# Kernel optimization log

Measured on AMD Instinct MI355X. Metric: run time of the kernel, lower is better.

The kernel has to match this reference:

```python
import jax, jax.numpy as jnp
import numpy as np

# SMPL-style 22-joint kinematic tree; parents[i] < i for i >= 2 as the module's loop requires.
PARENTS = np.array([-1, 0, 0, 0, 1, 2, 3, 4, 5, 6, 7, 8, 9, 9, 9, 12, 13, 14, 16, 17, 18, 19])
L, J, D6 = 65536, 22, 6


def cont6d_to_mat(d6):
    """6D continuous rotation -> 3x3 rotation matrix (Gram-Schmidt). Columns are b1,b2,b3."""
    a1, a2 = d6[..., :3], d6[..., 3:]
    b1 = a1 / jnp.maximum(jnp.linalg.norm(a1, axis=-1, keepdims=True), 1e-12)
    b2 = a2 - b1 * jnp.sum(b1 * a2, axis=-1, keepdims=True)
    b2 = b2 / jnp.maximum(jnp.linalg.norm(b2, axis=-1, keepdims=True), 1e-12)
    b3 = jnp.cross(b1, b2)
    return jnp.stack((b1, b2, b3), axis=-1)  # (..., 3, 3)


def setup_inputs() -> dict:
    key = jax.random.key(0)
    k1, k2 = jax.random.split(key)
    pred_series = jax.random.normal(k1, (L, J, D6), dtype=jnp.float32)
    offsets = 0.1 * jax.random.normal(k2, (J, 3), dtype=jnp.float32)  # bone offsets (buffer)
    return {"pred_series": pred_series, "offsets": offsets}


def reference(pred_series, offsets):
    # pred_series: (L, 22, 6) -> global positions (L, 22, 3)
    rot_mats = cont6d_to_mat(pred_series)          # (L, 22, 3, 3)

    # Cumulative root rotation: R_t = R_{t-1} @ delta_t, R_{-1} = I  (sequential scan over time)
    deltas = rot_mats[:, 1]                        # (L, 3, 3)
    def step(R, d):
        Rn = R @ d
        return Rn, Rn
    _, R = jax.lax.scan(step, jnp.eye(3, dtype=pred_series.dtype), deltas)  # (L, 3, 3)

    # Root translation: integrate rotated local velocities
    vel_local = pred_series[:, 0, :3]              # (L, 3)
    global_vel = jnp.einsum('tij,tj->ti', R, vel_local)
    root_pos = jnp.cumsum(global_vel, axis=0)      # (L, 3)

    # FK down the static tree, vectorized over time; unrolled over 22 joints (static).
    rots = [None] * J
    pos = [None] * J
    rots[0], pos[0] = R, root_pos
    rots[1] = R
    pos[1] = pos[0] + jnp.einsum('tij,j->ti', R, offsets[1])
    for i in range(2, J):
        p = int(PARENTS[i])
        rots[i] = jnp.einsum('tij,tjk->tik', rots[p], rot_mats[:, i])
        pos[i] = pos[p] + jnp.einsum('tij,j->ti', rots[p], offsets[i])
    return jnp.stack(pos, axis=1)                  # (L, 22, 3)
```

## Files before the change

### kernel.cpp

```cpp
#include <hip/hip_runtime.h>
#include <stdint.h>


#define LTOT 65536
#define ROW 132
#define P1B 256
#define NSCB (LTOT / P1B)

struct Aff { float A[9]; float b[3]; };

__device__ __forceinline__ void d6_to_mat(float a0, float a1, float a2,
                                          float a3, float a4, float a5,
                                          float R[9]) {
  float n1 = sqrtf(a0 * a0 + a1 * a1 + a2 * a2);
  float i1 = 1.0f / fmaxf(n1, 1e-12f);
  float b10 = a0 * i1, b11 = a1 * i1, b12 = a2 * i1;
  float d = b10 * a3 + b11 * a4 + b12 * a5;
  float c0 = a3 - d * b10, c1 = a4 - d * b11, c2 = a5 - d * b12;
  float n2 = sqrtf(c0 * c0 + c1 * c1 + c2 * c2);
  float i2 = 1.0f / fmaxf(n2, 1e-12f);
  float b20 = c0 * i2, b21 = c1 * i2, b22 = c2 * i2;
  float b30 = b11 * b22 - b12 * b21;
  float b31 = b12 * b20 - b10 * b22;
  float b32 = b10 * b21 - b11 * b20;
  R[0] = b10; R[1] = b20; R[2] = b30;
  R[3] = b11; R[4] = b21; R[5] = b31;
  R[6] = b12; R[7] = b22; R[8] = b32;
}

__device__ __forceinline__ void mat_mul(const float A[9], const float B[9], float C[9]) {
#pragma unroll
  for (int i = 0; i < 3; ++i)
#pragma unroll
    for (int j = 0; j < 3; ++j)
      C[i * 3 + j] = A[i * 3 + 0] * B[0 + j] + A[i * 3 + 1] * B[3 + j] + A[i * 3 + 2] * B[6 + j];
}

__device__ __forceinline__ void mat_vec(const float A[9], float x, float y, float z,
                                        float& ox, float& oy, float& oz) {
  ox = A[0] * x + A[1] * y + A[2] * z;
  oy = A[3] * x + A[4] * y + A[5] * z;
  oz = A[6] * x + A[7] * y + A[8] * z;
}

__device__ __forceinline__ void compose(const Aff& P, const Aff& T, Aff& O) {
  mat_mul(P.A, T.A, O.A);
  float bx, by, bz;
  mat_vec(P.A, T.b[0], T.b[1], T.b[2], bx, by, bz);
  O.b[0] = P.b[0] + bx; O.b[1] = P.b[1] + by; O.b[2] = P.b[2] + bz;
}

__device__ __forceinline__ void aff_identity(Aff& v) {
  v.A[0] = 1.f; v.A[1] = 0.f; v.A[2] = 0.f;
  v.A[3] = 0.f; v.A[4] = 1.f; v.A[5] = 0.f;
  v.A[6] = 0.f; v.A[7] = 0.f; v.A[8] = 1.f;
  v.b[0] = 0.f; v.b[1] = 0.f; v.b[2] = 0.f;
}

__device__ __forceinline__ void wave_scan(Aff& v, int lane) {
#pragma unroll
  for (int s = 1; s < 64; s <<= 1) {
    Aff u;
#pragma unroll
    for (int k = 0; k < 9; ++k) u.A[k] = __shfl_up(v.A[k], s, 64);
#pragma unroll
    for (int k = 0; k < 3; ++k) u.b[k] = __shfl_up(v.b[k], s, 64);
    if (lane >= s) { Aff t; compose(u, v, t); v = t; }
  }
}

__device__ __forceinline__ void elem_transform(const float* __restrict__ pred,
                                               int t, Aff& v) {
  const float4* q4 = (const float4*)(pred + (size_t)t * ROW);
  float4 qa = q4[0];
  float4 qb = q4[1];
  float4 qc = q4[2];
  d6_to_mat(qb.z, qb.w, qc.x, qc.y, qc.z, qc.w, v.A);
  mat_vec(v.A, qa.x, qa.y, qa.z, v.b[0], v.b[1], v.b[2]);
}

__global__ __launch_bounds__(P1B) void fk_agg(const float* __restrict__ pred,
                                              float* __restrict__ agg) {
  int tid = threadIdx.x;
  int t = blockIdx.x * P1B + tid;
  int lane = tid & 63, wid = tid >> 6;
  Aff v;
  elem_transform(pred, t, v);
  wave_scan(v, lane);
  __shared__ float sagg[P1B / 64][12];
  if (lane == 63) {
#pragma unroll
    for (int k = 0; k < 9; ++k) sagg[wid][k] = v.A[k];
#pragma unroll
    for (int k = 0; k < 3; ++k) sagg[wid][9 + k] = v.b[k];
  }
  __syncthreads();
  if (tid == P1B - 1) {
    Aff pre; aff_identity(pre);
    for (int w = 0; w < P1B / 64 - 1; ++w) {
      Aff g, t2;
#pragma unroll
      for (int k = 0; k < 9; ++k) g.A[k] = sagg[w][k];
#pragma unroll
      for (int k = 0; k < 3; ++k) g.b[k] = sagg[w][9 + k];
      compose(pre, g, t2); pre = t2;
    }
    Aff f; compose(pre, v, f);
    float4* a = (float4*)(agg + (size_t)blockIdx.x * 12);
    a[0] = make_float4(f.A[0], f.A[1], f.A[2], f.A[3]);
    a[1] = make_float4(f.A[4], f.A[5], f.A[6], f.A[7]);
    a[2] = make_float4(f.A[8], f.b[0], f.b[1], f.b[2]);
  }
}

struct Rowv { float2 a, b, c; };
__device__ __forceinline__ Rowv loadrow(const float* q, int j) {
  const float2* p = (const float2*)(q + j * 6);
  Rowv r; r.a = p[0]; r.b = p[1]; r.c = p[2]; return r;
}
__device__ __forceinline__ void rowmat(const Rowv& r, float M[9]) {
  d6_to_mat(r.a.x, r.a.y, r.b.x, r.b.y, r.c.x, r.c.y, M);
}
__device__ __forceinline__ void childp(const float* Rp, const float* offs, int j,
                                       float px, float py, float pz,
                                       float& ox, float& oy, float& oz,
                                       float* ob) {
  float dx, dy, dz;
  mat_vec(Rp, offs[j * 3], offs[j * 3 + 1], offs[j * 3 + 2], dx, dy, dz);
  ox = px + dx; oy = py + dy; oz = pz + dz;
  ob[j * 3] = ox; ob[j * 3 + 1] = oy; ob[j * 3 + 2] = oz;
}

__global__ __launch_bounds__(1024) void fk_main(const float* __restrict__ pred,
                                                const float* __restrict__ offs,
                                                const float* __restrict__ agg,
                                                float* __restrict__ out) {
  int x = threadIdx.x;
  int y = threadIdx.y;
  int z = threadIdx.z;
  int b = blockIdx.x;

  __shared__ float sagg1[4][12];
  __shared__ float sagg2[4][12];
  __shared__ float ebuf[12];
  __shared__ float sg[P1B][13];

  int tl = z * 64 + x;
  int t = b * P1B + tl;
  const float* q = pred + (size_t)t * ROW;
  float* ob = out + (size_t)t * 66;

  Rowv w0, w1, w2, w3, w4, w5, w6, w7, w8;
  if (y == 0) {
    w0 = loadrow(q, 4); w1 = loadrow(q, 7);
  } else if (y == 1) {
    w0 = loadrow(q, 2); w1 = loadrow(q, 5); w2 = loadrow(q, 8);
  } else if (y == 2) {
    w0 = loadrow(q, 3); w1 = loadrow(q, 6); w2 = loadrow(q, 9);
    w3 = loadrow(q, 12);
  } else {
    w0 = loadrow(q, 3); w1 = loadrow(q, 6); w2 = loadrow(q, 9);
    w3 = loadrow(q, 13); w4 = loadrow(q, 16); w5 = loadrow(q, 18);
    w6 = loadrow(q, 14); w7 = loadrow(q, 17); w8 = loadrow(q, 19);
  }

  int s = x + 64 * y;
  Aff v, f;
  Aff v2, incl;
  if (z == 0) {
    elem_transform(pred, b * P1B + s, v);
    wave_scan(v, x);
    if (x == 63) {
#pragma unroll
      for (int k = 0; k < 9; ++k) sagg1[y][k] = v.A[k];
#pragma unroll
      for (int k = 0; k < 3; ++k) sagg1[y][9 + k] = v.b[k];
    }
  } else if (z == 1) {
    const float4* a = (const float4*)(agg + (size_t)s * 12);
    float4 a0 = a[0], a1 = a[1], a2 = a[2];
    v2.A[0] = a0.x; v2.A[1] = a0.y; v2.A[2] = a0.z; v2.A[3] = a0.w;
    v2.A[4] = a1.x; v2.A[5] = a1.y; v2.A[6] = a1.z; v2.A[7] = a1.w;
    v2.A[8] = a2.x; v2.b[0] = a2.y; v2.b[1] = a2.z; v2.b[2] = a2.w;
    wave_scan(v2, x);
    if (x == 63) {
#pragma unroll
      for (int k = 0; k < 9; ++k) sagg2[y][k] = v2.A[k];
#pragma unroll
      for (int k = 0; k < 3; ++k) sagg2[y][9 + k] = v2.b[k];
    }
  }
  __syncthreads();

  if (z == 0) {
    Aff pre; aff_identity(pre);
    for (int w = 0; w < y; ++w) {
      Aff gg, t2;
#pragma unroll
      for (int k = 0; k < 9; ++k) gg.A[k] = sagg1[w][k];
#pragma unroll
      for (int k = 0; k < 3; ++k) gg.b[k] = sagg1[w][9 + k];
      compose(pre, gg, t2); pre = t2;
    }
    compose(pre, v, f);
  } else if (z == 1) {
    Aff pre; aff_identity(pre);
    for (int w = 0; w < y; ++w) {
      Aff gg, t2;
#pragma unroll
      for (int k = 0; k < 9; ++k) gg.A[k] = sagg2[w][k];
#pragma unroll
      for (int k = 0; k < 3; ++k) gg.b[k] = sagg2[w][9 + k];
      compose(pre, gg, t2); pre = t2;
    }
    compose(pre, v2, incl);
    if (s == b - 1) {
#pragma unroll
      for (int k = 0; k < 9; ++k) ebuf[k] = incl.A[k];
#pragma unroll
      for (int k = 0; k < 3; ++k) ebuf[9 + k] = incl.b[k];
    }
  }
  __syncthreads();

  if (z == 0) {
    Aff eb;
    if (b == 0) aff_identity(eb);
    else {
#pragma unroll
      for (int k = 0; k < 9; ++k) eb.A[k] = ebuf[k];
#pragma unroll
      for (int k = 0; k < 3; ++k) eb.b[k] = ebuf[9 + k];
    }
    Aff g; compose(eb, f, g);
#pragma unroll
    for (int k = 0; k < 9; ++k) sg[s][k] = g.A[k];
#pragma unroll
    for (int k = 0; k < 3; ++k) sg[s][9 + k] = g.b[k];
  }
  __syncthreads();

  float R[9];
#pragma unroll
  for (int k = 0; k < 9; ++k) R[k] = sg[tl][k];
  float px = sg[tl][9], py = sg[tl][10], pz = sg[tl][11];

  float M[9], ra[9], rb[9];
  if (y == 0) {
    ob[0] = px; ob[1] = py; ob[2] = pz;
    float p1x, p1y, p1z, p4x, p4y, p4z, p7x, p7y, p7z, dx, dy, dz;
    childp(R, offs, 1, px, py, pz, p1x, p1y, p1z, ob);
    childp(R, offs, 4, p1x, p1y, p1z, p4x, p4y, p4z, ob);
    rowmat(w0, M); mat_mul(R, M, ra);
    childp(ra, offs, 7, p4x, p4y, p4z, p7x, p7y, p7z, ob);
    rowmat(w1, M); mat_mul(ra, M, rb);
    childp(rb, offs, 10, p7x, p7y, p7z, dx, dy, dz, ob);
  } else if (y == 1) {
    float p2x, p2y, p2z, p5x, p5y, p5z, p8x, p8y, p8z, dx, dy, dz;
    childp(R, offs, 2, px, py, pz, p2x, p2y, p2z, ob);
    rowmat(w0, M); mat_mul(R, M, ra);
    childp(ra, offs, 5, p2x, p2y, p2z, p5x, p5y, p5z, ob);
    rowmat(w1, M); mat_mul(ra, M, rb);
    childp(rb, offs, 8, p5x, p5y, p5z, p8x, p8y, p8z, ob);
    rowmat(w2, M); mat_mul(rb, M, ra);
    childp(ra, offs, 11, p8x, p8y, p8z, dx, dy, dz, ob);
  } else if (y == 2) {
    float p3x, p3y, p3z, p6x, p6y, p6z, p9x, p9y, p9z;
    float p12x, p12y, p12z, dx, dy, dz;
    childp(R, offs, 3, px, py, pz, p3x, p3y, p3z, ob);
    rowmat(w0, M); mat_mul(R, M, ra);
    childp(ra, offs, 6, p3x, p3y, p3z, p6x, p6y, p6z, ob);
    rowmat(w1, M); mat_mul(ra, M, rb);
    childp(rb, offs, 9, p6x, p6y, p6z, p9x, p9y, p9z, ob);
    rowmat(w2, M); mat_mul(rb, M, ra);
    childp(ra, offs, 12, p9x, p9y, p9z, p12x, p12y, p12z, ob);
    rowmat(w3, M); mat_mul(ra, M, rb);
    childp(rb, offs, 15, p12x, p12y, p12z, dx, dy, dz, ob);
  } else {
    float p3x, p3y, p3z, p6x, p6y, p6z, p9x, p9y, p9z, dx, dy, dz;
    mat_vec(R, offs[9], offs[10], offs[11], dx, dy, dz);
    p3x = px + dx; p3y = py + dy; p3z = pz + dz;
    rowmat(w0, M); mat_mul(R, M, ra);
    mat_vec(ra, offs[18], offs[19], offs[20], dx, dy, dz);
    p6x = p3x + dx; p6y = p3y + dy; p6z = p3z + dz;
    rowmat(w1, M); mat_mul(ra, M, rb);
    mat_vec(rb, offs[27], offs[28], offs[29], dx, dy, dz);
    p9x = p6x + dx; p9y = p6y + dy; p9z = p6z + dz;
    rowmat(w2, M); mat_mul(rb, M, ra);
    float r9s[9];
#pragma unroll
    for (int k = 0; k < 9; ++k) r9s[k] = ra[k];
    float pAx, pAy, pAz, pBx, pBy, pBz, pCx, pCy, pCz;
    childp(r9s, offs, 13, p9x, p9y, p9z, pAx, pAy, pAz, ob);
    rowmat(w3, M); mat_mul(r9s, M, rb);
    childp(rb, offs, 16, pAx, pAy, pAz, pBx, pBy, pBz, ob);
    rowmat(w4, M); mat_mul(rb, M, ra);
    childp(ra, offs, 18, pBx, pBy, pBz, pCx, pCy, pCz, ob);
    rowmat(w5, M); mat_mul(ra, M, rb);
    childp(rb, offs, 20, pCx, pCy, pCz, dx, dy, dz, ob);
    childp(r9s, offs, 14, p9x, p9y, p9z, pAx, pAy, pAz, ob);
    rowmat(w6, M); mat_mul(r9s, M, rb);
    childp(rb, offs, 17, pAx, pAy, pAz, pBx, pBy, pBz, ob);
    rowmat(w7, M); mat_mul(rb, M, ra);
    childp(ra, offs, 19, pBx, pBy, pBz, pCx, pCy, pCz, ob);
    rowmat(w8, M); mat_mul(ra, M, rb);
    childp(rb, offs, 21, pCx, pCy, pCz, dx, dy, dz, ob);
  }
}

extern "C" void kernel_launch(void* const* d_in, const int* in_sizes, int n_in,
                              void* d_out, int out_size, void* d_ws, size_t ws_size,
                              hipStream_t stream) {
  const float* pred = (const float*)d_in[0];
  const float* offs = (const float*)d_in[1];
  float* out = (float*)d_out;
  float* agg = (float*)d_ws;

  fk_agg<<<NSCB, P1B, 0, stream>>>(pred, agg);
  fk_main<<<NSCB, dim3(64, 4, 4), 0, stream>>>(pred, offs, agg, out);
}
```

Measured before the change: 97.45 us.

## Fuse aggregate and main kernels into a single-pass scan with inter-block flags

Removes the separate aggregate kernel. Each block now publishes its own 256-step affine aggregate to workspace, then sets a release flag. Later blocks spin on the flags of all earlier blocks and scan those aggregates to get their prefix. This saves a launch and a second pass over the input rows. The cost is spin-waiting that assumes all earlier blocks are resident or scheduled first. The flags are never reset between calls, so a later call can see a stale flag from an earlier call and read stale aggregates.

```diff
diff --git a/kernel.cpp b/kernel.cpp
--- a/kernel.cpp
+++ b/kernel.cpp
@@ -6,6 +6,7 @@
 #define ROW 132
 #define P1B 256
 #define NSCB (LTOT / P1B)
+#define MAGIC 0x13579BDF
 
 struct Aff { float A[9]; float b[3]; };
 
@@ -79,40 +80,6 @@
   mat_vec(v.A, qa.x, qa.y, qa.z, v.b[0], v.b[1], v.b[2]);
 }
 
-__global__ __launch_bounds__(P1B) void fk_agg(const float* __restrict__ pred,
-                                              float* __restrict__ agg) {
-  int tid = threadIdx.x;
-  int t = blockIdx.x * P1B + tid;
-  int lane = tid & 63, wid = tid >> 6;
-  Aff v;
-  elem_transform(pred, t, v);
-  wave_scan(v, lane);
-  __shared__ float sagg[P1B / 64][12];
-  if (lane == 63) {
-#pragma unroll
-    for (int k = 0; k < 9; ++k) sagg[wid][k] = v.A[k];
-#pragma unroll
-    for (int k = 0; k < 3; ++k) sagg[wid][9 + k] = v.b[k];
-  }
-  __syncthreads();
-  if (tid == P1B - 1) {
-    Aff pre; aff_identity(pre);
-    for (int w = 0; w < P1B / 64 - 1; ++w) {
-      Aff g, t2;
-#pragma unroll
-      for (int k = 0; k < 9; ++k) g.A[k] = sagg[w][k];
-#pragma unroll
-      for (int k = 0; k < 3; ++k) g.b[k] = sagg[w][9 + k];
-      compose(pre, g, t2); pre = t2;
-    }
-    Aff f; compose(pre, v, f);
-    float4* a = (float4*)(agg + (size_t)blockIdx.x * 12);
-    a[0] = make_float4(f.A[0], f.A[1], f.A[2], f.A[3]);
-    a[1] = make_float4(f.A[4], f.A[5], f.A[6], f.A[7]);
-    a[2] = make_float4(f.A[8], f.b[0], f.b[1], f.b[2]);
-  }
-}
-
 struct Rowv { float2 a, b, c; };
 __device__ __forceinline__ Rowv loadrow(const float* q, int j) {
   const float2* p = (const float2*)(q + j * 6);
@@ -131,10 +98,11 @@
   ob[j * 3] = ox; ob[j * 3 + 1] = oy; ob[j * 3 + 2] = oz;
 }
 
-__global__ __launch_bounds__(1024) void fk_main(const float* __restrict__ pred,
-                                                const float* __restrict__ offs,
-                                                const float* __restrict__ agg,
-                                                float* __restrict__ out) {
+__global__ __launch_bounds__(1024) void fk_fused(const float* __restrict__ pred,
+                                                 const float* __restrict__ offs,
+                                                 float* __restrict__ agg,
+                                                 int* __restrict__ flags,
+                                                 float* __restrict__ out) {
   int x = threadIdx.x;
   int y = threadIdx.y;
   int z = threadIdx.z;
@@ -147,6 +115,7 @@
 
   int tl = z * 64 + x;
   int t = b * P1B + tl;
+  int s = x + 64 * y;
   const float* q = pred + (size_t)t * ROW;
   float* ob = out + (size_t)t * 66;
 
@@ -164,9 +133,7 @@
     w6 = loadrow(q, 14); w7 = loadrow(q, 17); w8 = loadrow(q, 19);
   }
 
-  int s = x + 64 * y;
-  Aff v, f;
-  Aff v2, incl;
+  Aff v;
   if (z == 0) {
     elem_transform(pred, b * P1B + s, v);
     wave_scan(v, x);
@@ -176,22 +143,10 @@
 #pragma unroll
       for (int k = 0; k < 3; ++k) sagg1[y][9 + k] = v.b[k];
     }
-  } else if (z == 1) {
-    const float4* a = (const float4*)(agg + (size_t)s * 12);
-    float4 a0 = a[0], a1 = a[1], a2 = a[2];
-    v2.A[0] = a0.x; v2.A[1] = a0.y; v2.A[2] = a0.z; v2.A[3] = a0.w;
-    v2.A[4] = a1.x; v2.A[5] = a1.y; v2.A[6] = a1.z; v2.A[7] = a1.w;
-    v2.A[8] = a2.x; v2.b[0] = a2.y; v2.b[1] = a2.z; v2.b[2] = a2.w;
-    wave_scan(v2, x);
-    if (x == 63) {
-#pragma unroll
-      for (int k = 0; k < 9; ++k) sagg2[y][k] = v2.A[k];
-#pragma unroll
-      for (int k = 0; k < 3; ++k) sagg2[y][9 + k] = v2.b[k];
-    }
   }
   __syncthreads();
 
+  Aff v2;
   if (z == 0) {
     Aff pre; aff_identity(pre);
     for (int w = 0; w < y; ++w) {
@@ -202,8 +157,45 @@
       for (int k = 0; k < 3; ++k) gg.b[k] = sagg1[w][9 + k];
       compose(pre, gg, t2); pre = t2;
     }
-    compose(pre, v, f);
+    Aff f; compose(pre, v, f);
+#pragma unroll
+    for (int k = 0; k < 9; ++k) sg[s][k] = f.A[k];
+#pragma unroll
+    for (int k = 0; k < 3; ++k) sg[s][9 + k] = f.b[k];
+    if (s == P1B - 1) {
+      float4* a = (float4*)(agg + (size_t)b * 12);
+      a[0] = make_float4(f.A[0], f.A[1], f.A[2], f.A[3]);
+      a[1] = make_float4(f.A[4], f.A[5], f.A[6], f.A[7]);
+      a[2] = make_float4(f.A[8], f.b[0], f.b[1], f.b[2]);
+      __threadfence();
+      __hip_atomic_store(&flags[b], MAGIC, __ATOMIC_RELEASE,
+                         __HIP_MEMORY_SCOPE_AGENT);
+    }
   } else if (z == 1) {
+    if (s < b) {
+      while (__hip_atomic_load(&flags[s], __ATOMIC_ACQUIRE,
+                               __HIP_MEMORY_SCOPE_AGENT) != MAGIC) {
+        __builtin_amdgcn_s_sleep(1);
+      }
+      const float4* a = (const float4*)(agg + (size_t)s * 12);
+      float4 a0 = a[0], a1 = a[1], a2 = a[2];
+      v2.A[0] = a0.x; v2.A[1] = a0.y; v2.A[2] = a0.z; v2.A[3] = a0.w;
+      v2.A[4] = a1.x; v2.A[5] = a1.y; v2.A[6] = a1.z; v2.A[7] = a1.w;
+      v2.A[8] = a2.x; v2.b[0] = a2.y; v2.b[1] = a2.z; v2.b[2] = a2.w;
+    } else {
+      aff_identity(v2);
+    }
+    wave_scan(v2, x);
+    if (x == 63) {
+#pragma unroll
+      for (int k = 0; k < 9; ++k) sagg2[y][k] = v2.A[k];
+#pragma unroll
+      for (int k = 0; k < 3; ++k) sagg2[y][9 + k] = v2.b[k];
+    }
+  }
+  __syncthreads();
+
+  if (z == 1 && b > 0 && s == b - 1) {
     Aff pre; aff_identity(pre);
     for (int w = 0; w < y; ++w) {
       Aff gg, t2;
@@ -213,37 +205,30 @@
       for (int k = 0; k < 3; ++k) gg.b[k] = sagg2[w][9 + k];
       compose(pre, gg, t2); pre = t2;
     }
-    compose(pre, v2, incl);
-    if (s == b - 1) {
-#pragma unroll
-      for (int k = 0; k < 9; ++k) ebuf[k] = incl.A[k];
-#pragma unroll
-      for (int k = 0; k < 3; ++k) ebuf[9 + k] = incl.b[k];
-    }
+    Aff incl; compose(pre, v2, incl);
+#pragma unroll
+    for (int k = 0; k < 9; ++k) ebuf[k] = incl.A[k];
+#pragma unroll
+    for (int k = 0; k < 3; ++k) ebuf[9 + k] = incl.b[k];
   }
   __syncthreads();
 
-  if (z == 0) {
-    Aff eb;
-    if (b == 0) aff_identity(eb);
-    else {
-#pragma unroll
-      for (int k = 0; k < 9; ++k) eb.A[k] = ebuf[k];
-#pragma unroll
-      for (int k = 0; k < 3; ++k) eb.b[k] = ebuf[9 + k];
-    }
-    Aff g; compose(eb, f, g);
-#pragma unroll
-    for (int k = 0; k < 9; ++k) sg[s][k] = g.A[k];
-#pragma unroll
-    for (int k = 0; k < 3; ++k) sg[s][9 + k] = g.b[k];
-  }
-  __syncthreads();
-
-  float R[9];
-#pragma unroll
-  for (int k = 0; k < 9; ++k) R[k] = sg[tl][k];
-  float px = sg[tl][9], py = sg[tl][10], pz = sg[tl][11];
+  Aff eb;
+  if (b == 0) aff_identity(eb);
+  else {
+#pragma unroll
+    for (int k = 0; k < 9; ++k) eb.A[k] = ebuf[k];
+#pragma unroll
+    for (int k = 0; k < 3; ++k) eb.b[k] = ebuf[9 + k];
+  }
+  Aff fl;
+#pragma unroll
+  for (int k = 0; k < 9; ++k) fl.A[k] = sg[tl][k];
+#pragma unroll
+  for (int k = 0; k < 3; ++k) fl.b[k] = sg[tl][9 + k];
+  Aff g; compose(eb, fl, g);
+  const float* R = g.A;
+  float px = g.b[0], py = g.b[1], pz = g.b[2];
 
   float M[9], ra[9], rb[9];
   if (y == 0) {
@@ -315,7 +300,7 @@
   const float* offs = (const float*)d_in[1];
   float* out = (float*)d_out;
   float* agg = (float*)d_ws;
-
-  fk_agg<<<NSCB, P1B, 0, stream>>>(pred, agg);
-  fk_main<<<NSCB, dim3(64, 4, 4), 0, stream>>>(pred, offs, agg, out);
-}
+  int* flags = (int*)((char*)d_ws + 16384);
+
+  fk_fused<<<NSCB, dim3(64, 4, 4), 0, stream>>>(pred, offs, agg, flags, out);
+}
```

After: 135.9 us. 39.5% more time.

## Rebalance FK branches across waves and remove a block barrier

Applied to the files above, without the earlier changes.

The two 4-joint leaf chains (13/16/18/20 and 14/17/19/21) were all done by the y==3 wave. They are now split between y==0 and y==3, which take the joint-9 frame from the y==2 wave through shared memory after a barrier. Composing each block's prefix with the previous block's carry is now done per thread from shared memory, which removes one barrier. Only the single thread that produces the carry runs the second prefix compose. Row loads are deferred to where they are used, which cuts register pressure but gives up early load prefetch and adds a 256x13 shared buffer.

```diff
diff --git a/kernel.cpp b/kernel.cpp
--- a/kernel.cpp
+++ b/kernel.cpp
@@ -144,29 +144,15 @@
   __shared__ float sagg2[4][12];
   __shared__ float ebuf[12];
   __shared__ float sg[P1B][13];
+  __shared__ float s9[P1B][13];
 
   int tl = z * 64 + x;
   int t = b * P1B + tl;
+  int s = x + 64 * y;
   const float* q = pred + (size_t)t * ROW;
   float* ob = out + (size_t)t * 66;
 
-  Rowv w0, w1, w2, w3, w4, w5, w6, w7, w8;
-  if (y == 0) {
-    w0 = loadrow(q, 4); w1 = loadrow(q, 7);
-  } else if (y == 1) {
-    w0 = loadrow(q, 2); w1 = loadrow(q, 5); w2 = loadrow(q, 8);
-  } else if (y == 2) {
-    w0 = loadrow(q, 3); w1 = loadrow(q, 6); w2 = loadrow(q, 9);
-    w3 = loadrow(q, 12);
-  } else {
-    w0 = loadrow(q, 3); w1 = loadrow(q, 6); w2 = loadrow(q, 9);
-    w3 = loadrow(q, 13); w4 = loadrow(q, 16); w5 = loadrow(q, 18);
-    w6 = loadrow(q, 14); w7 = loadrow(q, 17); w8 = loadrow(q, 19);
-  }
-
-  int s = x + 64 * y;
-  Aff v, f;
-  Aff v2, incl;
+  Aff v, v2;
   if (z == 0) {
     elem_transform(pred, b * P1B + s, v);
     wave_scan(v, x);
@@ -202,8 +188,12 @@
       for (int k = 0; k < 3; ++k) gg.b[k] = sagg1[w][9 + k];
       compose(pre, gg, t2); pre = t2;
     }
-    compose(pre, v, f);
-  } else if (z == 1) {
+    Aff f; compose(pre, v, f);
+#pragma unroll
+    for (int k = 0; k < 9; ++k) sg[s][k] = f.A[k];
+#pragma unroll
+    for (int k = 0; k < 3; ++k) sg[s][9 + k] = f.b[k];
+  } else if (z == 1 && b > 0 && s == b - 1) {
     Aff pre; aff_identity(pre);
     for (int w = 0; w < y; ++w) {
       Aff gg, t2;
@@ -213,37 +203,30 @@
       for (int k = 0; k < 3; ++k) gg.b[k] = sagg2[w][9 + k];
       compose(pre, gg, t2); pre = t2;
     }
-    compose(pre, v2, incl);
-    if (s == b - 1) {
-#pragma unroll
-      for (int k = 0; k < 9; ++k) ebuf[k] = incl.A[k];
-#pragma unroll
-      for (int k = 0; k < 3; ++k) ebuf[9 + k] = incl.b[k];
-    }
-  }
-  __syncthreads();
-
-  if (z == 0) {
-    Aff eb;
-    if (b == 0) aff_identity(eb);
-    else {
-#pragma unroll
-      for (int k = 0; k < 9; ++k) eb.A[k] = ebuf[k];
-#pragma unroll
-      for (int k = 0; k < 3; ++k) eb.b[k] = ebuf[9 + k];
-    }
-    Aff g; compose(eb, f, g);
-#pragma unroll
-    for (int k = 0; k < 9; ++k) sg[s][k] = g.A[k];
-#pragma unroll
-    for (int k = 0; k < 3; ++k) sg[s][9 + k] = g.b[k];
-  }
-  __syncthreads();
-
-  float R[9];
-#pragma unroll
-  for (int k = 0; k < 9; ++k) R[k] = sg[tl][k];
-  float px = sg[tl][9], py = sg[tl][10], pz = sg[tl][11];
+    Aff incl; compose(pre, v2, incl);
+#pragma unroll
+    for (int k = 0; k < 9; ++k) ebuf[k] = incl.A[k];
+#pragma unroll
+    for (int k = 0; k < 3; ++k) ebuf[9 + k] = incl.b[k];
+  }
+  __syncthreads();
+
+  Aff eb;
+  if (b == 0) aff_identity(eb);
+  else {
+#pragma unroll
+    for (int k = 0; k < 9; ++k) eb.A[k] = ebuf[k];
+#pragma unroll
+    for (int k = 0; k < 3; ++k) eb.b[k] = ebuf[9 + k];
+  }
+  Aff fl;
+#pragma unroll
+  for (int k = 0; k < 9; ++k) fl.A[k] = sg[tl][k];
+#pragma unroll
+  for (int k = 0; k < 3; ++k) fl.b[k] = sg[tl][9 + k];
+  Aff g; compose(eb, fl, g);
+  const float* R = g.A;
+  float px = g.b[0], py = g.b[1], pz = g.b[2];
 
   float M[9], ra[9], rb[9];
   if (y == 0) {
@@ -251,60 +234,53 @@
     float p1x, p1y, p1z, p4x, p4y, p4z, p7x, p7y, p7z, dx, dy, dz;
     childp(R, offs, 1, px, py, pz, p1x, p1y, p1z, ob);
     childp(R, offs, 4, p1x, p1y, p1z, p4x, p4y, p4z, ob);
-    rowmat(w0, M); mat_mul(R, M, ra);
+    Rowv w = loadrow(q, 4); rowmat(w, M); mat_mul(R, M, ra);
     childp(ra, offs, 7, p4x, p4y, p4z, p7x, p7y, p7z, ob);
-    rowmat(w1, M); mat_mul(ra, M, rb);
+    w = loadrow(q, 7); rowmat(w, M); mat_mul(ra, M, rb);
     childp(rb, offs, 10, p7x, p7y, p7z, dx, dy, dz, ob);
   } else if (y == 1) {
     float p2x, p2y, p2z, p5x, p5y, p5z, p8x, p8y, p8z, dx, dy, dz;
     childp(R, offs, 2, px, py, pz, p2x, p2y, p2z, ob);
-    rowmat(w0, M); mat_mul(R, M, ra);
+    Rowv w = loadrow(q, 2); rowmat(w, M); mat_mul(R, M, ra);
     childp(ra, offs, 5, p2x, p2y, p2z, p5x, p5y, p5z, ob);
-    rowmat(w1, M); mat_mul(ra, M, rb);
+    w = loadrow(q, 5); rowmat(w, M); mat_mul(ra, M, rb);
     childp(rb, offs, 8, p5x, p5y, p5z, p8x, p8y, p8z, ob);
-    rowmat(w2, M); mat_mul(rb, M, ra);
+    w = loadrow(q, 8); rowmat(w, M); mat_mul(rb, M, ra);
     childp(ra, offs, 11, p8x, p8y, p8z, dx, dy, dz, ob);
   } else if (y == 2) {
     float p3x, p3y, p3z, p6x, p6y, p6z, p9x, p9y, p9z;
     float p12x, p12y, p12z, dx, dy, dz;
     childp(R, offs, 3, px, py, pz, p3x, p3y, p3z, ob);
-    rowmat(w0, M); mat_mul(R, M, ra);
+    Rowv w = loadrow(q, 3); rowmat(w, M); mat_mul(R, M, ra);
     childp(ra, offs, 6, p3x, p3y, p3z, p6x, p6y, p6z, ob);
-    rowmat(w1, M); mat_mul(ra, M, rb);
+    w = loadrow(q, 6); rowmat(w, M); mat_mul(ra, M, rb);
     childp(rb, offs, 9, p6x, p6y, p6z, p9x, p9y, p9z, ob);
-    rowmat(w2, M); mat_mul(rb, M, ra);
+    w = loadrow(q, 9); rowmat(w, M); mat_mul(rb, M, ra);
+#pragma unroll
+    for (int k = 0; k < 9; ++k) s9[tl][k] = ra[k];
+    s9[tl][9] = p9x; s9[tl][10] = p9y; s9[tl][11] = p9z;
     childp(ra, offs, 12, p9x, p9y, p9z, p12x, p12y, p12z, ob);
-    rowmat(w3, M); mat_mul(ra, M, rb);
+    w = loadrow(q, 12); rowmat(w, M); mat_mul(ra, M, rb);
     childp(rb, offs, 15, p12x, p12y, p12z, dx, dy, dz, ob);
-  } else {
-    float p3x, p3y, p3z, p6x, p6y, p6z, p9x, p9y, p9z, dx, dy, dz;
-    mat_vec(R, offs[9], offs[10], offs[11], dx, dy, dz);
-    p3x = px + dx; p3y = py + dy; p3z = pz + dz;
-    rowmat(w0, M); mat_mul(R, M, ra);
-    mat_vec(ra, offs[18], offs[19], offs[20], dx, dy, dz);
-    p6x = p3x + dx; p6y = p3y + dy; p6z = p3z + dz;
-    rowmat(w1, M); mat_mul(ra, M, rb);
-    mat_vec(rb, offs[27], offs[28], offs[29], dx, dy, dz);
-    p9x = p6x + dx; p9y = p6y + dy; p9z = p6z + dz;
-    rowmat(w2, M); mat_mul(rb, M, ra);
+  }
+  __syncthreads();
+
+  if (y == 0 || y == 3) {
     float r9s[9];
 #pragma unroll
-    for (int k = 0; k < 9; ++k) r9s[k] = ra[k];
-    float pAx, pAy, pAz, pBx, pBy, pBz, pCx, pCy, pCz;
-    childp(r9s, offs, 13, p9x, p9y, p9z, pAx, pAy, pAz, ob);
-    rowmat(w3, M); mat_mul(r9s, M, rb);
-    childp(rb, offs, 16, pAx, pAy, pAz, pBx, pBy, pBz, ob);
-    rowmat(w4, M); mat_mul(rb, M, ra);
-    childp(ra, offs, 18, pBx, pBy, pBz, pCx, pCy, pCz, ob);
-    rowmat(w5, M); mat_mul(ra, M, rb);
-    childp(rb, offs, 20, pCx, pCy, pCz, dx, dy, dz, ob);
-    childp(r9s, offs, 14, p9x, p9y, p9z, pAx, pAy, pAz, ob);
-    rowmat(w6, M); mat_mul(r9s, M, rb);
-    childp(rb, offs, 17, pAx, pAy, pAz, pBx, pBy, pBz, ob);
-    rowmat(w7, M); mat_mul(rb, M, ra);
-    childp(ra, offs, 19, pBx, pBy, pBz, pCx, pCy, pCz, ob);
-    rowmat(w8, M); mat_mul(ra, M, rb);
-    childp(rb, offs, 21, pCx, pCy, pCz, dx, dy, dz, ob);
+    for (int k = 0; k < 9; ++k) r9s[k] = s9[tl][k];
+    float p9x = s9[tl][9], p9y = s9[tl][10], p9z = s9[tl][11];
+    int jA, jB, jC, jD;
+    if (y == 3) { jA = 13; jB = 16; jC = 18; jD = 20; }
+    else        { jA = 14; jB = 17; jC = 19; jD = 21; }
+    float pAx, pAy, pAz, pBx, pBy, pBz, pCx, pCy, pCz, dx, dy, dz;
+    childp(r9s, offs, jA, p9x, p9y, p9z, pAx, pAy, pAz, ob);
+    Rowv w = loadrow(q, jA); rowmat(w, M); mat_mul(r9s, M, rb);
+    childp(rb, offs, jB, pAx, pAy, pAz, pBx, pBy, pBz, ob);
+    w = loadrow(q, jB); rowmat(w, M); mat_mul(rb, M, ra);
+    childp(ra, offs, jC, pBx, pBy, pBz, pCx, pCy, pCz, ob);
+    w = loadrow(q, jC); rowmat(w, M); mat_mul(ra, M, rb);
+    childp(rb, offs, jD, pCx, pCy, pCz, dx, dy, dz, ob);
   }
 }
 
```

Measured after the change: 97.07 us. Within noise of the previous version (-0.4%).
